# Performance work log

Measured on AMD Instinct MI355X. Metric: run time of the kernel, lower is better.

Reference implementation:

```python
import jax, jax.numpy as jnp
import numpy as np

DIM, DEPTH, HEADS, MLP = 1024, 6, 16, 4096
HEAD_DIM = DIM // HEADS
SCALE = DIM ** -0.5  # NOTE: original uses full dim, not head_dim
EPS = 1e-5


def _layernorm(x, g, b):
    m = jnp.mean(x, axis=-1, keepdims=True)
    v = jnp.mean((x - m) ** 2, axis=-1, keepdims=True)
    return (x - m) * jax.lax.rsqrt(v + EPS) * g + b


def setup_inputs() -> dict:
    key = jax.random.key(0)
    ks = jax.random.split(key, 12)
    d = DEPTH
    s_qkv = (DIM * 3) ** -0.5  # ~kaiming-ish scale, values only need to be plausible
    inp = {
        "x": jax.random.normal(ks[0], (2, 2048, DIM), dtype=jnp.float32),
        "Wqkv": jax.random.normal(ks[1], (d, DIM, 3 * DIM), dtype=jnp.float32) * s_qkv,
        "Wout": jax.random.normal(ks[2], (d, DIM, DIM), dtype=jnp.float32) * (DIM ** -0.5),
        "bout": jnp.zeros((d, DIM), dtype=jnp.float32),
        "ln1_g": jnp.ones((d, DIM), dtype=jnp.float32),
        "ln1_b": jnp.zeros((d, DIM), dtype=jnp.float32),
        "ln2_g": jnp.ones((d, DIM), dtype=jnp.float32),
        "ln2_b": jnp.zeros((d, DIM), dtype=jnp.float32),
        "W1": jax.random.normal(ks[3], (d, DIM, MLP), dtype=jnp.float32) * (DIM ** -0.5),
        "b1": jnp.zeros((d, MLP), dtype=jnp.float32),
        "W2": jax.random.normal(ks[4], (d, MLP, DIM), dtype=jnp.float32) * (MLP ** -0.5),
        "b2": jnp.zeros((d, DIM), dtype=jnp.float32),
    }
    return inp


def _transformer(x, Wqkv, Wout, bout, ln1_g, ln1_b, ln2_g, ln2_b, W1, b1, W2, b2):
    b, n, _ = x.shape

    def layer(h, p):
        wqkv, wout, bo, g1, bb1, g2, bb2, w1, bf1, w2, bf2 = p
        # --- attention block (Residual(PreNorm(SelfAttention))) ---
        y = _layernorm(h, g1, bb1)
        qkv = y @ wqkv                                   # [b, n, 3*dim]
        qkv = qkv.reshape(b, n, 3, HEADS, HEAD_DIM)
        q, k, v = [jnp.transpose(qkv[:, :, i], (0, 2, 1, 3)) for i in range(3)]  # [b,h,n,d]
        dots = jnp.einsum("bhid,bhjd->bhij", q, k) * SCALE
        attn = jax.nn.softmax(dots, axis=-1)
        o = jnp.einsum("bhij,bhjd->bhid", attn, v)       # [b,h,n,d]
        o = jnp.transpose(o, (0, 2, 1, 3)).reshape(b, n, DIM)
        h = h + (o @ wout + bo)
        # --- FFN block (Residual(PreNorm(FeedForward))) ---
        y = _layernorm(h, g2, bb2)
        y = jax.nn.gelu(y @ w1 + bf1, approximate=False) @ w2 + bf2
        return h + y, None

    params = (Wqkv, Wout, bout, ln1_g, ln1_b, ln2_g, ln2_b, W1, b1, W2, b2)
    out, _ = jax.lax.scan(layer, x, params)
    return out


def reference(x, Wqkv, Wout, bout, ln1_g, ln1_b, ln2_g, ln2_b, W1, b1, W2, b2):
    return _transformer(x, Wqkv, Wout, bout, ln1_g, ln1_b, ln2_g, ln2_b, W1, b1, W2, b2)
```

## Files before the change

### kernel.cpp

```cpp
#include <hip/hip_runtime.h>
#include <hip/hip_bf16.h>
#include <math.h>

typedef __attribute__((__ext_vector_type__(8))) __bf16 bf16x8;
typedef __attribute__((__ext_vector_type__(4))) float f32x4;

#define DIMQ 1024
#define SEQ 2048
#define NTOK 4096
#define HEADS 16
#define HD 64
#define MLPD 4096
#define DEPTH 6

__device__ __forceinline__ void gl_lds16(const __hip_bfloat16* g, __hip_bfloat16* l) {
  __builtin_amdgcn_global_load_lds((const __attribute__((address_space(1))) void*)(g),
                                   (__attribute__((address_space(3))) void*)(l), 16, 0, 0);
}

__device__ __forceinline__ unsigned cvtpk_bf16(float lo, float hi) {
  unsigned r;
  asm("v_cvt_pk_bf16_f32 %0, %1, %2" : "=v"(r) : "v"(lo), "v"(hi));
  return r;
}

__global__ __launch_bounds__(256) void ln_kernel(const float* __restrict__ h,
                                                 const float* __restrict__ g,
                                                 const float* __restrict__ bta,
                                                 __hip_bfloat16* __restrict__ y) {
  int row = blockIdx.x;
  int t = threadIdx.x;
  const float4* src = (const float4*)(h + (size_t)row * DIMQ);
  float4 xv = src[t];
  float s = xv.x + xv.y + xv.z + xv.w;
  float ss = xv.x * xv.x + xv.y * xv.y + xv.z * xv.z + xv.w * xv.w;
#pragma unroll
  for (int off = 32; off > 0; off >>= 1) {
    s += __shfl_xor(s, off);
    ss += __shfl_xor(ss, off);
  }
  __shared__ float red[8];
  int wid = t >> 6;
  if ((t & 63) == 0) { red[wid] = s; red[4 + wid] = ss; }
  __syncthreads();
  s = red[0] + red[1] + red[2] + red[3];
  ss = red[4] + red[5] + red[6] + red[7];
  float mean = s * (1.0f / DIMQ);
  float var = ss * (1.0f / DIMQ) - mean * mean;
  float rstd = rsqrtf(var + 1e-5f);
  float4 gv = ((const float4*)g)[t];
  float4 bv = ((const float4*)bta)[t];
  __hip_bfloat16* dst = y + (size_t)row * DIMQ + t * 4;
  dst[0] = __float2bfloat16((xv.x - mean) * rstd * gv.x + bv.x);
  dst[1] = __float2bfloat16((xv.y - mean) * rstd * gv.y + bv.y);
  dst[2] = __float2bfloat16((xv.z - mean) * rstd * gv.z + bv.z);
  dst[3] = __float2bfloat16((xv.w - mean) * rstd * gv.w + bv.w);
}

__global__ __launch_bounds__(256)
void transpose_cast4(const float* __restrict__ s0, const float* __restrict__ s1,
                     const float* __restrict__ s2, const float* __restrict__ s3,
                     __hip_bfloat16* __restrict__ d0, __hip_bfloat16* __restrict__ d1,
                     __hip_bfloat16* __restrict__ d2, __hip_bfloat16* __restrict__ d3) {
  __shared__ float t[32][33];
  int tb = blockIdx.x;
  const float* src;
  __hip_bfloat16* dst;
  int K, N;
  if (tb < 3072) { src = s0; dst = d0; K = 1024; N = 3072; }
  else if (tb < 4096) { tb -= 3072; src = s1; dst = d1; K = 1024; N = 1024; }
  else if (tb < 8192) { tb -= 4096; src = s2; dst = d2; K = 1024; N = 4096; }
  else { tb -= 8192; src = s3; dst = d3; K = 4096; N = 1024; }
  int ntx = N >> 5;
  int n0 = (tb % ntx) * 32, k0 = (tb / ntx) * 32;
  int tx = threadIdx.x, ty = threadIdx.y;
#pragma unroll
  for (int i = 0; i < 32; i += 8)
    t[ty + i][tx] = src[(size_t)(k0 + ty + i) * N + n0 + tx];
  __syncthreads();
#pragma unroll
  for (int i = 0; i < 32; i += 8)
    dst[(size_t)(n0 + ty + i) * K + k0 + tx] = __float2bfloat16(t[tx][ty + i]);
}

template <int EPI>
__global__ __launch_bounds__(256)
void gemm128(const __hip_bfloat16* __restrict__ A, const __hip_bfloat16* __restrict__ BT,
             const float* __restrict__ bias, void* __restrict__ outp, void* __restrict__ outp2,
             int M, int N, int K, int gpx) {
  __shared__ __hip_bfloat16 As[128][64];
  __shared__ __hip_bfloat16 Bs[128][64];
  int bid = blockIdx.x;
  int xcd = bid & 7, jb = bid >> 3;
  int nt = xcd * gpx + (jb % gpx), mt = jb / gpx;
  int m0 = mt * 128, n0 = nt * 128;
  int tid = threadIdx.x;
  int lane = tid & 63, wid = tid >> 6;
  int l16 = lane & 15, quad = lane >> 4;
  int wm = (wid >> 1) * 64, wn = (wid & 1) * 64;
  int srsub = lane >> 3;
  int sg = (lane & 7) ^ srsub;
  f32x4 acc[4][4] = {};
  for (int kt = 0; kt < K; kt += 64) {
    __syncthreads();
#pragma unroll
    for (int s = 0; s < 4; ++s) {
      int r0 = (wid * 4 + s) * 8;
      gl_lds16(A + (size_t)(m0 + r0 + srsub) * K + kt + sg * 8, &As[r0][0]);
      gl_lds16(BT + (size_t)(n0 + r0 + srsub) * K + kt + sg * 8, &Bs[r0][0]);
    }
    __syncthreads();
#pragma unroll
    for (int ks = 0; ks < 2; ++ks) {
      bf16x8 af[4], bfr[4];
      int p = (ks * 4 + quad) ^ (l16 & 7);
#pragma unroll
      for (int i = 0; i < 4; ++i) af[i] = *(const bf16x8*)&As[wm + i * 16 + l16][p * 8];
#pragma unroll
      for (int j = 0; j < 4; ++j) bfr[j] = *(const bf16x8*)&Bs[wn + j * 16 + l16][p * 8];
#pragma unroll
      for (int i = 0; i < 4; ++i)
#pragma unroll
        for (int j = 0; j < 4; ++j)
          acc[i][j] = __builtin_amdgcn_mfma_f32_16x16x32_bf16(af[i], bfr[j], acc[i][j], 0, 0, 0);
    }
  }
#pragma unroll
  for (int j = 0; j < 4; ++j) {
    int col = n0 + wn + j * 16 + l16;
    if (EPI == 1) {
      float bv = bias[col];
#pragma unroll
      for (int i = 0; i < 4; ++i) {
#pragma unroll
        for (int r = 0; r < 4; ++r) {
          int row = m0 + wm + i * 16 + quad * 4 + r;
          float v = acc[i][j][r] + bv;
          v = 0.5f * v * (1.0f + erff(v * 0.70710678118654752f));
          ((__hip_bfloat16*)outp)[(size_t)row * N + col] = __float2bfloat16(v);
        }
      }
    } else {
      int which = col >> 10;
      int head = (col >> 6) & 15;
      int d = col & 63;
      if (which < 2) {
#pragma unroll
        for (int i = 0; i < 4; ++i) {
#pragma unroll
          for (int r = 0; r < 4; ++r) {
            int row = m0 + wm + i * 16 + quad * 4 + r;
            size_t dst = (((size_t)which * 32 + (row >> 11) * 16 + head) * SEQ + (row & 2047)) * HD + d;
            ((__hip_bfloat16*)outp)[dst] = __float2bfloat16(acc[i][j][r]);
          }
        }
      } else {
        int bh2 = ((m0 >> 11) << 4) + head;
        unsigned short* vrow = (unsigned short*)outp2 + ((size_t)bh2 * HD + d) * SEQ;
        int nb = (m0 & 2047) + wm + quad * 4;
#pragma unroll
        for (int i = 0; i < 4; ++i) {
          uint2 pk;
          pk.x = cvtpk_bf16(acc[i][j][0], acc[i][j][1]);
          pk.y = cvtpk_bf16(acc[i][j][2], acc[i][j][3]);
          *(uint2*)(vrow + nb + i * 16) = pk;
        }
      }
    }
  }
}

__global__ __launch_bounds__(256, 5)
void gemm64_res(const __hip_bfloat16* __restrict__ A, const __hip_bfloat16* __restrict__ BT,
                const float* __restrict__ bias, float* __restrict__ h,
                int M, int N, int K, int gpx) {
  __shared__ __hip_bfloat16 As[128][64];
  __shared__ __hip_bfloat16 Bs[64][64];
  int bid = blockIdx.x;
  int xcd = bid & 7, jb = bid >> 3;
  int nt = xcd * gpx + (jb % gpx), mt = jb / gpx;
  int m0 = mt * 128, n0 = nt * 64;
  int tid = threadIdx.x;
  int lane = tid & 63, wid = tid >> 6;
  int l16 = lane & 15, quad = lane >> 4;
  int wm = (wid >> 1) * 64, wn = (wid & 1) * 32;
  int srsub = lane >> 3;
  int sg = (lane & 7) ^ srsub;
  f32x4 acc[4][2] = {};
  for (int kt = 0; kt < K; kt += 64) {
    __syncthreads();
#pragma unroll
    for (int s = 0; s < 4; ++s) {
      int r0 = (wid * 4 + s) * 8;
      gl_lds16(A + (size_t)(m0 + r0 + srsub) * K + kt + sg * 8, &As[r0][0]);
    }
#pragma unroll
    for (int s = 0; s < 2; ++s) {
      int r0 = (wid * 2 + s) * 8;
      gl_lds16(BT + (size_t)(n0 + r0 + srsub) * K + kt + sg * 8, &Bs[r0][0]);
    }
    __syncthreads();
#pragma unroll
    for (int ks = 0; ks < 2; ++ks) {
      bf16x8 af[4], bfr[2];
      int p = (ks * 4 + quad) ^ (l16 & 7);
#pragma unroll
      for (int i = 0; i < 4; ++i) af[i] = *(const bf16x8*)&As[wm + i * 16 + l16][p * 8];
#pragma unroll
      for (int j = 0; j < 2; ++j) bfr[j] = *(const bf16x8*)&Bs[wn + j * 16 + l16][p * 8];
#pragma unroll
      for (int i = 0; i < 4; ++i)
#pragma unroll
        for (int j = 0; j < 2; ++j)
          acc[i][j] = __builtin_amdgcn_mfma_f32_16x16x32_bf16(af[i], bfr[j], acc[i][j], 0, 0, 0);
    }
  }
#pragma unroll
  for (int j = 0; j < 2; ++j) {
    int col = n0 + wn + j * 16 + l16;
    float bv = bias[col];
#pragma unroll
    for (int i = 0; i < 4; ++i) {
#pragma unroll
      for (int r = 0; r < 4; ++r) {
        int row = m0 + wm + i * 16 + quad * 4 + r;
        size_t idx = (size_t)row * N + col;
        h[idx] = h[idx] + acc[i][j][r] + bv;
      }
    }
  }
}

__global__ __launch_bounds__(256)
void attn_kernel(const __hip_bfloat16* __restrict__ qkvb, const __hip_bfloat16* __restrict__ vT,
                 __hip_bfloat16* __restrict__ o) {
  __shared__ __hip_bfloat16 Ks[64][64];
  __shared__ __hip_bfloat16 Vs[64][64];
  __shared__ __hip_bfloat16 Ps[4][16][68];
  int bh = blockIdx.y;
  int b = bh >> 4;
  int tid = threadIdx.x;
  int wid = tid >> 6, lane = tid & 63;
  int l16 = lane & 15, quad = lane >> 4;
  int qrow = blockIdx.x * 64 + wid * 16 + l16;
  const __hip_bfloat16* qp = qkvb + ((size_t)bh * SEQ + qrow) * HD;
  bf16x8 qf0 = *(const bf16x8*)(qp + quad * 8);
  bf16x8 qf1 = *(const bf16x8*)(qp + 32 + quad * 8);
  f32x4 oacc[4] = {};
  float lsum[4] = {0.0f, 0.0f, 0.0f, 0.0f};
  int srsub = lane >> 3;
  int sg = (lane & 7) ^ srsub;
  const __hip_bfloat16* kbase = qkvb + (size_t)(32 + bh) * SEQ * HD;
  const __hip_bfloat16* vbase = vT + (size_t)bh * HD * SEQ;
  const float c1 = 0.045084220027780106f;
  for (int kb = 0; kb < SEQ; kb += 64) {
    __syncthreads();
    {
      int r0 = wid * 16, r1 = wid * 16 + 8;
      gl_lds16(kbase + (size_t)(kb + r0 + srsub) * HD + sg * 8, &Ks[r0][0]);
      gl_lds16(kbase + (size_t)(kb + r1 + srsub) * HD + sg * 8, &Ks[r1][0]);
      gl_lds16(vbase + (size_t)(r0 + srsub) * SEQ + kb + sg * 8, &Vs[r0][0]);
      gl_lds16(vbase + (size_t)(r1 + srsub) * SEQ + kb + sg * 8, &Vs[r1][0]);
    }
    __syncthreads();
    f32x4 sc[4];
    int p0 = quad ^ (l16 & 7);
    int p1 = (4 + quad) ^ (l16 & 7);
#pragma unroll
    for (int c = 0; c < 4; ++c) {
      int r = c * 16 + l16;
      bf16x8 k0 = *(const bf16x8*)&Ks[r][p0 * 8];
      bf16x8 k1 = *(const bf16x8*)&Ks[r][p1 * 8];
      f32x4 z = {};
      z = __builtin_amdgcn_mfma_f32_16x16x32_bf16(qf0, k0, z, 0, 0, 0);
      z = __builtin_amdgcn_mfma_f32_16x16x32_bf16(qf1, k1, z, 0, 0, 0);
      sc[c] = z;
    }
#pragma unroll
    for (int r = 0; r < 4; ++r) {
      float psum = 0.0f;
#pragma unroll
      for (int c = 0; c < 4; ++c) {
        float p = exp2f(sc[c][r] * c1);
        psum += p;
        Ps[wid][quad * 4 + r][c * 16 + l16] = __float2bfloat16(p);
      }
      lsum[r] += psum;
    }
    asm volatile("s_waitcnt lgkmcnt(0)" ::: "memory");
    bf16x8 pf0 = *(const bf16x8*)&Ps[wid][l16][quad * 8];
    bf16x8 pf1 = *(const bf16x8*)&Ps[wid][l16][32 + quad * 8];
#pragma unroll
    for (int f = 0; f < 4; ++f) {
      int r = f * 16 + l16;
      bf16x8 v0 = *(const bf16x8*)&Vs[r][p0 * 8];
      bf16x8 v1 = *(const bf16x8*)&Vs[r][p1 * 8];
      oacc[f] = __builtin_amdgcn_mfma_f32_16x16x32_bf16(pf0, v0, oacc[f], 0, 0, 0);
      oacc[f] = __builtin_amdgcn_mfma_f32_16x16x32_bf16(pf1, v1, oacc[f], 0, 0, 0);
    }
  }
#pragma unroll
  for (int r = 0; r < 4; ++r) {
#pragma unroll
    for (int off = 1; off < 16; off <<= 1) lsum[r] += __shfl_xor(lsum[r], off);
  }
  int h = bh & 15;
  int orow = b * SEQ + blockIdx.x * 64 + wid * 16 + quad * 4;
#pragma unroll
  for (int r = 0; r < 4; ++r) {
    float inv = 1.0f / lsum[r];
#pragma unroll
    for (int f = 0; f < 4; ++f) {
      o[(size_t)(orow + r) * DIMQ + h * HD + f * 16 + l16] = __float2bfloat16(oacc[f][r] * inv);
    }
  }
}

extern "C" void kernel_launch(void* const* d_in, const int* in_sizes, int n_in,
                              void* d_out, int out_size, void* d_ws, size_t ws_size,
                              hipStream_t stream) {
  const float* x = (const float*)d_in[0];
  const float* Wqkv = (const float*)d_in[1];
  const float* Wout = (const float*)d_in[2];
  const float* bout = (const float*)d_in[3];
  const float* ln1g = (const float*)d_in[4];
  const float* ln1b = (const float*)d_in[5];
  const float* ln2g = (const float*)d_in[6];
  const float* ln2b = (const float*)d_in[7];
  const float* W1 = (const float*)d_in[8];
  const float* b1 = (const float*)d_in[9];
  const float* W2 = (const float*)d_in[10];
  const float* b2 = (const float*)d_in[11];
  float* h = (float*)d_out;

  char* ws = (char*)d_ws;
  __hip_bfloat16* wqkvT = (__hip_bfloat16*)ws; ws += (size_t)3072 * 1024 * 2;
  __hip_bfloat16* woutT = (__hip_bfloat16*)ws; ws += (size_t)1024 * 1024 * 2;
  __hip_bfloat16* w1T = (__hip_bfloat16*)ws;   ws += (size_t)4096 * 1024 * 2;
  __hip_bfloat16* w2T = (__hip_bfloat16*)ws;   ws += (size_t)1024 * 4096 * 2;
  __hip_bfloat16* ybuf = (__hip_bfloat16*)ws;  ws += (size_t)NTOK * 1024 * 2;
  __hip_bfloat16* qkvb = (__hip_bfloat16*)ws;  ws += (size_t)NTOK * 3072 * 2;
  __hip_bfloat16* vTb = (__hip_bfloat16*)ws;   ws += (size_t)32 * HD * SEQ * 2;
  __hip_bfloat16* obuf = (__hip_bfloat16*)ws;  ws += (size_t)NTOK * 1024 * 2;
  __hip_bfloat16* actb = (__hip_bfloat16*)ws;  ws += (size_t)NTOK * MLPD * 2;

  hipMemcpyAsync(h, x, (size_t)out_size * sizeof(float), hipMemcpyDeviceToDevice, stream);

  dim3 tb(32, 8);
  for (int l = 0; l < DEPTH; ++l) {
    transpose_cast4<<<12288, tb, 0, stream>>>(
        Wqkv + (size_t)l * 1024 * 3072, Wout + (size_t)l * 1024 * 1024,
        W1 + (size_t)l * 1024 * 4096, W2 + (size_t)l * 4096 * 1024,
        wqkvT, woutT, w1T, w2T);

    ln_kernel<<<NTOK, 256, 0, stream>>>(h, ln1g + l * 1024, ln1b + l * 1024, ybuf);
    gemm128<3><<<768, 256, 0, stream>>>(ybuf, wqkvT, nullptr, qkvb, vTb, NTOK, 3072, 1024, 3);
    attn_kernel<<<dim3(SEQ / 64, 32), 256, 0, stream>>>(qkvb, vTb, obuf);
    gemm64_res<<<512, 256, 0, stream>>>(obuf, woutT, bout + l * 1024, h, NTOK, 1024, 1024, 2);

    ln_kernel<<<NTOK, 256, 0, stream>>>(h, ln2g + l * 1024, ln2b + l * 1024, ybuf);
    gemm128<1><<<1024, 256, 0, stream>>>(ybuf, w1T, b1 + l * 4096, actb, nullptr, NTOK, 4096, 1024, 4);
    gemm64_res<<<512, 256, 0, stream>>>(actb, w2T, b2 + l * 1024, h, NTOK, 1024, 4096, 2);
  }
}
```

Baseline: 2.010 ms.

## Rewrite attention with 32x32 MFMA, in-register P, double-buffered K/V

The attention kernel moves from 16x16x32 to 32x32x16 MFMA and computes transposed scores (K·Q^T). That layout lets the exp'd probabilities stay in registers, repacked with v_permlane32_swap instead of going through an LDS round trip. K/V tiles are double-buffered with async global-to-LDS loads and waited on with vmcnt, so loads overlap compute. Each block now covers 128 queries with 32 per wave, and MFMA sections get raised s_setprio. The risks are higher register pressure, lower occupancy from half as many blocks, and subtle correctness issues in the swizzle and the wrap-around prefetch.

```diff
diff --git a/kernel.cpp b/kernel.cpp
--- a/kernel.cpp
+++ b/kernel.cpp
@@ -4,6 +4,7 @@
 
 typedef __attribute__((__ext_vector_type__(8))) __bf16 bf16x8;
 typedef __attribute__((__ext_vector_type__(4))) float f32x4;
+typedef __attribute__((__ext_vector_type__(16))) float f32x16;
 
 #define DIMQ 1024
 #define SEQ 2048
@@ -234,84 +235,107 @@
 __global__ __launch_bounds__(256)
 void attn_kernel(const __hip_bfloat16* __restrict__ qkvb, const __hip_bfloat16* __restrict__ vT,
                  __hip_bfloat16* __restrict__ o) {
-  __shared__ __hip_bfloat16 Ks[64][64];
-  __shared__ __hip_bfloat16 Vs[64][64];
-  __shared__ __hip_bfloat16 Ps[4][16][68];
+  __shared__ __hip_bfloat16 Ks[2][64][64];
+  __shared__ __hip_bfloat16 Vs[2][64][64];
   int bh = blockIdx.y;
-  int b = bh >> 4;
+  int b = bh >> 4, head = bh & 15;
   int tid = threadIdx.x;
   int wid = tid >> 6, lane = tid & 63;
-  int l16 = lane & 15, quad = lane >> 4;
-  int qrow = blockIdx.x * 64 + wid * 16 + l16;
-  const __hip_bfloat16* qp = qkvb + ((size_t)bh * SEQ + qrow) * HD;
-  bf16x8 qf0 = *(const bf16x8*)(qp + quad * 8);
-  bf16x8 qf1 = *(const bf16x8*)(qp + 32 + quad * 8);
-  f32x4 oacc[4] = {};
-  float lsum[4] = {0.0f, 0.0f, 0.0f, 0.0f};
+  int l32 = lane & 31, hh = lane >> 5;
+  int q0 = blockIdx.x * 128 + wid * 32;
+  const __hip_bfloat16* qp = qkvb + ((size_t)bh * SEQ + q0 + l32) * HD + hh * 8;
+  bf16x8 qf[4];
+#pragma unroll
+  for (int k16 = 0; k16 < 4; ++k16) qf[k16] = *(const bf16x8*)(qp + k16 * 16);
+
+  f32x16 oaccT[2] = {};
+  float lsum = 0.0f;
   int srsub = lane >> 3;
   int sg = (lane & 7) ^ srsub;
   const __hip_bfloat16* kbase = qkvb + (size_t)(32 + bh) * SEQ * HD;
   const __hip_bfloat16* vbase = vT + (size_t)bh * HD * SEQ;
   const float c1 = 0.045084220027780106f;
+
+  int r0 = wid * 16, r1 = wid * 16 + 8;
+#define STAGE_KV(bi, kb)                                                          \
+  do {                                                                            \
+    gl_lds16(kbase + (size_t)((kb) + r0 + srsub) * HD + sg * 8, &Ks[bi][r0][0]);  \
+    gl_lds16(kbase + (size_t)((kb) + r1 + srsub) * HD + sg * 8, &Ks[bi][r1][0]);  \
+    gl_lds16(vbase + (size_t)(r0 + srsub) * SEQ + (kb) + sg * 8, &Vs[bi][r0][0]); \
+    gl_lds16(vbase + (size_t)(r1 + srsub) * SEQ + (kb) + sg * 8, &Vs[bi][r1][0]); \
+  } while (0)
+
+  STAGE_KV(0, 0);
+  STAGE_KV(1, 64);
+
   for (int kb = 0; kb < SEQ; kb += 64) {
-    __syncthreads();
-    {
-      int r0 = wid * 16, r1 = wid * 16 + 8;
-      gl_lds16(kbase + (size_t)(kb + r0 + srsub) * HD + sg * 8, &Ks[r0][0]);
-      gl_lds16(kbase + (size_t)(kb + r1 + srsub) * HD + sg * 8, &Ks[r1][0]);
-      gl_lds16(vbase + (size_t)(r0 + srsub) * SEQ + kb + sg * 8, &Vs[r0][0]);
-      gl_lds16(vbase + (size_t)(r1 + srsub) * SEQ + kb + sg * 8, &Vs[r1][0]);
-    }
-    __syncthreads();
-    f32x4 sc[4];
-    int p0 = quad ^ (l16 & 7);
-    int p1 = (4 + quad) ^ (l16 & 7);
-#pragma unroll
-    for (int c = 0; c < 4; ++c) {
-      int r = c * 16 + l16;
-      bf16x8 k0 = *(const bf16x8*)&Ks[r][p0 * 8];
-      bf16x8 k1 = *(const bf16x8*)&Ks[r][p1 * 8];
-      f32x4 z = {};
-      z = __builtin_amdgcn_mfma_f32_16x16x32_bf16(qf0, k0, z, 0, 0, 0);
-      z = __builtin_amdgcn_mfma_f32_16x16x32_bf16(qf1, k1, z, 0, 0, 0);
-      sc[c] = z;
-    }
-#pragma unroll
-    for (int r = 0; r < 4; ++r) {
-      float psum = 0.0f;
-#pragma unroll
-      for (int c = 0; c < 4; ++c) {
-        float p = exp2f(sc[c][r] * c1);
-        psum += p;
-        Ps[wid][quad * 4 + r][c * 16 + l16] = __float2bfloat16(p);
-      }
-      lsum[r] += psum;
-    }
-    asm volatile("s_waitcnt lgkmcnt(0)" ::: "memory");
-    bf16x8 pf0 = *(const bf16x8*)&Ps[wid][l16][quad * 8];
-    bf16x8 pf1 = *(const bf16x8*)&Ps[wid][l16][32 + quad * 8];
-#pragma unroll
-    for (int f = 0; f < 4; ++f) {
-      int r = f * 16 + l16;
-      bf16x8 v0 = *(const bf16x8*)&Vs[r][p0 * 8];
-      bf16x8 v1 = *(const bf16x8*)&Vs[r][p1 * 8];
-      oacc[f] = __builtin_amdgcn_mfma_f32_16x16x32_bf16(pf0, v0, oacc[f], 0, 0, 0);
-      oacc[f] = __builtin_amdgcn_mfma_f32_16x16x32_bf16(pf1, v1, oacc[f], 0, 0, 0);
-    }
-  }
-#pragma unroll
-  for (int r = 0; r < 4; ++r) {
-#pragma unroll
-    for (int off = 1; off < 16; off <<= 1) lsum[r] += __shfl_xor(lsum[r], off);
-  }
-  int h = bh & 15;
-  int orow = b * SEQ + blockIdx.x * 64 + wid * 16 + quad * 4;
-#pragma unroll
-  for (int r = 0; r < 4; ++r) {
-    float inv = 1.0f / lsum[r];
-#pragma unroll
-    for (int f = 0; f < 4; ++f) {
-      o[(size_t)(orow + r) * DIMQ + h * HD + f * 16 + l16] = __float2bfloat16(oacc[f][r] * inv);
+    int cur = (kb >> 6) & 1;
+    asm volatile("s_waitcnt vmcnt(4)" ::: "memory");
+    asm volatile("s_barrier" ::: "memory");
+#pragma unroll
+    for (int s = 0; s < 2; ++s) {
+      f32x16 z = {};
+      __builtin_amdgcn_s_setprio(1);
+#pragma unroll
+      for (int k16 = 0; k16 < 4; ++k16) {
+        int krow = s * 32 + l32;
+        int cc = k16 * 2 + hh;
+        bf16x8 kf = *(const bf16x8*)&Ks[cur][krow][(cc ^ (krow & 7)) * 8];
+        z = __builtin_amdgcn_mfma_f32_32x32x16_bf16(kf, qf[k16], z, 0, 0, 0);
+      }
+      __builtin_amdgcn_s_setprio(0);
+      unsigned dw0, dw1, dw2, dw3, dw4, dw5, dw6, dw7;
+      {
+        float pa, pb;
+        pa = exp2f(z[0] * c1);  pb = exp2f(z[1] * c1);  lsum += pa + pb; dw0 = cvtpk_bf16(pa, pb);
+        pa = exp2f(z[2] * c1);  pb = exp2f(z[3] * c1);  lsum += pa + pb; dw1 = cvtpk_bf16(pa, pb);
+        pa = exp2f(z[4] * c1);  pb = exp2f(z[5] * c1);  lsum += pa + pb; dw2 = cvtpk_bf16(pa, pb);
+        pa = exp2f(z[6] * c1);  pb = exp2f(z[7] * c1);  lsum += pa + pb; dw3 = cvtpk_bf16(pa, pb);
+        pa = exp2f(z[8] * c1);  pb = exp2f(z[9] * c1);  lsum += pa + pb; dw4 = cvtpk_bf16(pa, pb);
+        pa = exp2f(z[10] * c1); pb = exp2f(z[11] * c1); lsum += pa + pb; dw5 = cvtpk_bf16(pa, pb);
+        pa = exp2f(z[12] * c1); pb = exp2f(z[13] * c1); lsum += pa + pb; dw6 = cvtpk_bf16(pa, pb);
+        pa = exp2f(z[14] * c1); pb = exp2f(z[15] * c1); lsum += pa + pb; dw7 = cvtpk_bf16(pa, pb);
+      }
+      asm volatile("v_permlane32_swap_b32 %0, %1" : "+v"(dw0), "+v"(dw2));
+      asm volatile("v_permlane32_swap_b32 %0, %1" : "+v"(dw1), "+v"(dw3));
+      asm volatile("v_permlane32_swap_b32 %0, %1" : "+v"(dw4), "+v"(dw6));
+      asm volatile("v_permlane32_swap_b32 %0, %1" : "+v"(dw5), "+v"(dw7));
+      union PU { unsigned u[4]; bf16x8 v; };
+      PU p0u, p1u;
+      p0u.u[0] = dw0; p0u.u[1] = dw1; p0u.u[2] = dw2; p0u.u[3] = dw3;
+      p1u.u[0] = dw4; p1u.u[1] = dw5; p1u.u[2] = dw6; p1u.u[3] = dw7;
+      __builtin_amdgcn_s_setprio(1);
+#pragma unroll
+      for (int c = 0; c < 2; ++c) {
+        bf16x8 pf = (c == 0) ? p0u.v : p1u.v;
+        int cc = s * 4 + c * 2 + hh;
+#pragma unroll
+        for (int dblk = 0; dblk < 2; ++dblk) {
+          int dr = dblk * 32 + l32;
+          bf16x8 vf = *(const bf16x8*)&Vs[cur][dr][(cc ^ (dr & 7)) * 8];
+          oaccT[dblk] = __builtin_amdgcn_mfma_f32_32x32x16_bf16(vf, pf, oaccT[dblk], 0, 0, 0);
+        }
+      }
+      __builtin_amdgcn_s_setprio(0);
+    }
+    asm volatile("s_barrier" ::: "memory");
+    int nk = kb + 128;
+    if (nk >= SEQ) nk = 0;
+    STAGE_KV(cur, nk);
+  }
+#undef STAGE_KV
+
+  lsum += __shfl_xor(lsum, 32);
+  float inv = 1.0f / lsum;
+  __hip_bfloat16* orow = o + ((size_t)b * SEQ + q0 + l32) * DIMQ + head * HD;
+#pragma unroll
+  for (int dblk = 0; dblk < 2; ++dblk) {
+#pragma unroll
+    for (int g2 = 0; g2 < 4; ++g2) {
+      uint2 pk;
+      pk.x = cvtpk_bf16(oaccT[dblk][g2 * 4 + 0] * inv, oaccT[dblk][g2 * 4 + 1] * inv);
+      pk.y = cvtpk_bf16(oaccT[dblk][g2 * 4 + 2] * inv, oaccT[dblk][g2 * 4 + 3] * inv);
+      *(uint2*)(orow + dblk * 32 + g2 * 8 + 4 * hh) = pk;
     }
   }
 }
@@ -355,7 +379,7 @@
 
     ln_kernel<<<NTOK, 256, 0, stream>>>(h, ln1g + l * 1024, ln1b + l * 1024, ybuf);
     gemm128<3><<<768, 256, 0, stream>>>(ybuf, wqkvT, nullptr, qkvb, vTb, NTOK, 3072, 1024, 3);
-    attn_kernel<<<dim3(SEQ / 64, 32), 256, 0, stream>>>(qkvb, vTb, obuf);
+    attn_kernel<<<dim3(SEQ / 128, 32), 256, 0, stream>>>(qkvb, vTb, obuf);
     gemm64_res<<<512, 256, 0, stream>>>(obuf, woutT, bout + l * 1024, h, NTOK, 1024, 1024, 2);
 
     ln_kernel<<<NTOK, 256, 0, stream>>>(h, ln2g + l * 1024, ln2b + l * 1024, ybuf);
```

Result: faster. 1.927 ms (-4.1%).
